# Optimization experiments

Hardware: AMD Instinct MI355X
Metric: run time of the kernel (lower is better)

The kernel has to match this reference:

```python
import jax, jax.numpy as jnp
import numpy as np

B, S, D, E, R = 8, 4096, 768, 8, 8

def setup_inputs() -> dict:
    key = jax.random.key(0)
    ks = jax.random.split(key, 9)
    sc = 0.02
    return {
        "x":  jax.random.normal(ks[0], (B, S, D), dtype=jnp.float32),
        "Wd": jax.random.normal(ks[1], (E, D, R), dtype=jnp.float32) * sc,
        "bd": jax.random.normal(ks[2], (E, R), dtype=jnp.float32) * sc,
        "Wm": jax.random.normal(ks[3], (E, R, R), dtype=jnp.float32) * sc,
        "bm": jax.random.normal(ks[4], (E, R), dtype=jnp.float32) * sc,
        "Wu": jax.random.normal(ks[5], (E, R, D), dtype=jnp.float32) * sc,
        "bu": jax.random.normal(ks[6], (E, D), dtype=jnp.float32) * sc,
        "Wg": jax.random.normal(ks[7], (D, E), dtype=jnp.float32) * sc,
        "bg": jax.random.normal(ks[8], (E,), dtype=jnp.float32) * sc,
    }

def reference(x, Wd, bd, Wm, bm, Wu, bu, Wg, bg):
    # Gating: softmax over experts. [B,S,E]
    gate = jax.nn.softmax(jnp.einsum('bsd,de->bse', x, Wg) + bg, axis=-1)
    # All experts batched as 3D GEMMs (dropout = identity, eval mode).
    h = jnp.einsum('bsd,edr->bser', x, Wd) + bd            # [B,S,E,R] down
    h = jnp.einsum('bser,erq->bseq', h, Wm) + bm           # [B,S,E,R] mid
    up = jnp.einsum('bser,erd->bsed', h, Wu) + bu          # [B,S,E,D] up
    # Weighted sum over experts.
    return jnp.einsum('bse,bsed->bsd', gate, up)
```

## Files before the change

kernel.cpp:

```cpp
#include <hip/hip_runtime.h>
#include <stdint.h>


typedef short bf16x8 __attribute__((ext_vector_type(8)));
typedef float f32x4 __attribute__((ext_vector_type(4)));

static __device__ __forceinline__ unsigned short f2bf(float f) {
  union { float f; uint32_t u; } v; v.f = f;
  return (unsigned short)((v.u + 0x7fffu + ((v.u >> 16) & 1u)) >> 16);
}

__global__ void prep_weights(const float* __restrict__ Wd, const float* __restrict__ Wg,
                             const float* __restrict__ Wu, const float* __restrict__ bu,
                             unsigned short* __restrict__ w1f, unsigned short* __restrict__ w2f) {
  int tid = blockIdx.x * 256 + threadIdx.x;
  const int N1 = 24 * 5 * 64 * 8;
  if (tid < N1) {
    int i    = tid & 7;
    int lane = (tid >> 3) & 63;
    int fk   = tid >> 9;
    int f = fk % 5, K0 = fk / 5;
    int k = K0 * 32 + (lane >> 4) * 8 + i;
    int j = f * 16 + (lane & 15);
    float val = 0.f;
    if (j < 64)      val = Wd[(size_t)(j >> 3) * 6144 + (size_t)k * 8 + (j & 7)];
    else if (j < 72) val = Wg[(size_t)k * 8 + (j - 64)];
    w1f[tid] = f2bf(val);
  } else {
    int t2 = tid - N1;
    if (t2 >= 48 * 3 * 64 * 8) return;
    int i    = t2 & 7;
    int lane = (t2 >> 3) & 63;
    int tk   = t2 >> 9;
    int K0 = tk % 3, T = tk / 3;
    int k = K0 * 32 + (lane >> 4) * 8 + i;
    int n = T * 16 + (lane & 15);
    float val = 0.f;
    if (k < 64)      val = Wu[(size_t)(k >> 3) * 6144 + (size_t)(k & 7) * 768 + n];
    else if (k < 72) val = bu[(size_t)(k - 64) * 768 + n];
    w2f[t2] = f2bf(val);
  }
}

__global__ __launch_bounds__(256, 4) void moba_fused(
    const float* __restrict__ x,
    const float* __restrict__ bd, const float* __restrict__ Wm,
    const float* __restrict__ bm, const float* __restrict__ bg,
    const unsigned short* __restrict__ w1f, const unsigned short* __restrict__ w2f,
    float* __restrict__ out) {
  __shared__ float Hs[2][32][81];
  __shared__ unsigned int g2s[32][52];

  const int tidx = threadIdx.x;
  const int lane = tidx & 63;
  const int wave = tidx >> 6;
  const int tg   = wave >> 1;
  const int kh   = wave & 1;
  const int arow = lane & 15;
  const int kgrp = lane >> 4;
  const int tok0 = blockIdx.x * 32;

  {
    const float* xrow = x + (size_t)(tok0 + tg * 16 + arow) * 768 + kh * 384 + kgrp * 8;
    f32x4 acc0 = {0,0,0,0}, acc1 = {0,0,0,0}, acc2 = {0,0,0,0}, acc3 = {0,0,0,0}, acc4 = {0,0,0,0};
    const bf16x8* w1v = (const bf16x8*)w1f + (size_t)(kh * 12) * 320 + lane;

    float4 xa[4][2];
    #pragma unroll
    for (int i = 0; i < 4; i++) {
      xa[i][0] = *(const float4*)(xrow + i * 32);
      xa[i][1] = *(const float4*)(xrow + i * 32 + 4);
    }
    #pragma unroll
    for (int i = 0; i < 12; i++) {
      float4 a0 = xa[i & 3][0];
      float4 a1 = xa[i & 3][1];
      if (i + 4 < 12) {
        xa[i & 3][0] = *(const float4*)(xrow + (i + 4) * 32);
        xa[i & 3][1] = *(const float4*)(xrow + (i + 4) * 32 + 4);
      }
      bf16x8 af;
      af[0] = (short)f2bf(a0.x); af[1] = (short)f2bf(a0.y);
      af[2] = (short)f2bf(a0.z); af[3] = (short)f2bf(a0.w);
      af[4] = (short)f2bf(a1.x); af[5] = (short)f2bf(a1.y);
      af[6] = (short)f2bf(a1.z); af[7] = (short)f2bf(a1.w);
      const bf16x8* bb = w1v + i * 320;
      acc0 = __builtin_amdgcn_mfma_f32_16x16x32_bf16(af, bb[0],   acc0, 0, 0, 0);
      acc1 = __builtin_amdgcn_mfma_f32_16x16x32_bf16(af, bb[64],  acc1, 0, 0, 0);
      acc2 = __builtin_amdgcn_mfma_f32_16x16x32_bf16(af, bb[128], acc2, 0, 0, 0);
      acc3 = __builtin_amdgcn_mfma_f32_16x16x32_bf16(af, bb[192], acc3, 0, 0, 0);
      acc4 = __builtin_amdgcn_mfma_f32_16x16x32_bf16(af, bb[256], acc4, 0, 0, 0);
    }
    int hr = tg * 16 + kgrp * 4;
    #pragma unroll
    for (int r = 0; r < 4; r++) {
      Hs[kh][hr + r][arow]      = acc0[r];
      Hs[kh][hr + r][16 + arow] = acc1[r];
      Hs[kh][hr + r][32 + arow] = acc2[r];
      Hs[kh][hr + r][48 + arow] = acc3[r];
      Hs[kh][hr + r][64 + arow] = acc4[r];
    }
  }
  __syncthreads();

  if (tidx < 128) {
    int t = tidx >> 2;
    int c = tidx & 3;
    float lg[8];
    float m = -1e30f;
    #pragma unroll
    for (int e = 0; e < 8; e++) {
      lg[e] = Hs[0][t][64 + e] + Hs[1][t][64 + e] + bg[e];
      m = fmaxf(m, lg[e]);
    }
    float den = 0.f;
    #pragma unroll
    for (int e = 0; e < 8; e++) { lg[e] = __expf(lg[e] - m); den += lg[e]; }
    float inv = 1.f / den;
    #pragma unroll
    for (int ee = 0; ee < 2; ee++) {
      int e = c * 2 + ee;
      float gate = lg[e] * inv;
      float h[8];
      #pragma unroll
      for (int r = 0; r < 8; r++)
        h[r] = Hs[0][t][e * 8 + r] + Hs[1][t][e * 8 + r] + bd[e * 8 + r];
      #pragma unroll
      for (int q = 0; q < 8; q += 2) {
        float h2a = bm[e * 8 + q], h2b = bm[e * 8 + q + 1];
        #pragma unroll
        for (int r = 0; r < 8; r++) {
          h2a += h[r] * Wm[e * 64 + r * 8 + q];
          h2b += h[r] * Wm[e * 64 + r * 8 + q + 1];
        }
        g2s[t][e * 4 + (q >> 1)] =
            (unsigned)f2bf(gate * h2a) | ((unsigned)f2bf(gate * h2b) << 16);
      }
    }
    g2s[t][32 + c] = (unsigned)f2bf(lg[c * 2] * inv) | ((unsigned)f2bf(lg[c * 2 + 1] * inv) << 16);
    g2s[t][36 + c * 3 + 0] = 0;
    g2s[t][36 + c * 3 + 1] = 0;
    g2s[t][36 + c * 3 + 2] = 0;
  }
  __syncthreads();

  bf16x8 a2_0 = *(const bf16x8*)&g2s[tg * 16 + arow][kgrp * 4];
  bf16x8 a2_1 = *(const bf16x8*)&g2s[tg * 16 + arow][16 + kgrp * 4];
  bf16x8 a2_2 = *(const bf16x8*)&g2s[tg * 16 + arow][32 + kgrp * 4];
  const bf16x8* w2v = (const bf16x8*)w2f + (size_t)(kh * 24) * 192 + lane;
  float* orow = out + (size_t)(tok0 + tg * 16 + kgrp * 4) * 768 + arow + kh * 384;

  bf16x8 pb[4][3];
  #pragma unroll
  for (int d = 0; d < 4; d++) {
    pb[d][0] = w2v[d * 192];
    pb[d][1] = w2v[d * 192 + 64];
    pb[d][2] = w2v[d * 192 + 128];
  }
  #pragma unroll
  for (int j = 0; j < 24; j++) {
    bf16x8 b0 = pb[j & 3][0], b1 = pb[j & 3][1], b2 = pb[j & 3][2];
    if (j + 4 < 24) {
      pb[j & 3][0] = w2v[(j + 4) * 192];
      pb[j & 3][1] = w2v[(j + 4) * 192 + 64];
      pb[j & 3][2] = w2v[(j + 4) * 192 + 128];
    }
    f32x4 c2 = {0,0,0,0};
    c2 = __builtin_amdgcn_mfma_f32_16x16x32_bf16(a2_0, b0, c2, 0, 0, 0);
    c2 = __builtin_amdgcn_mfma_f32_16x16x32_bf16(a2_1, b1, c2, 0, 0, 0);
    c2 = __builtin_amdgcn_mfma_f32_16x16x32_bf16(a2_2, b2, c2, 0, 0, 0);
    #pragma unroll
    for (int r = 0; r < 4; r++)
      orow[(size_t)r * 768 + j * 16] = c2[r];
  }
}

extern "C" void kernel_launch(void* const* d_in, const int* in_sizes, int n_in,
                              void* d_out, int out_size, void* d_ws, size_t ws_size,
                              hipStream_t stream) {
  const float* x  = (const float*)d_in[0];
  const float* Wd = (const float*)d_in[1];
  const float* bd = (const float*)d_in[2];
  const float* Wm = (const float*)d_in[3];
  const float* bm = (const float*)d_in[4];
  const float* Wu = (const float*)d_in[5];
  const float* bu = (const float*)d_in[6];
  const float* Wg = (const float*)d_in[7];
  const float* bg = (const float*)d_in[8];
  unsigned short* w1f = (unsigned short*)d_ws;
  unsigned short* w2f = w1f + 61440;

  prep_weights<<<528, 256, 0, stream>>>(Wd, Wg, Wu, bu, w1f, w2f);
  moba_fused<<<1024, 256, 0, stream>>>(x, bd, Wm, bm, bg, w1f, w2f, (float*)d_out);
}
```

Before: 57.72 us.

## Halve tokens per block, split K four ways across waves, use nontemporal stores

Each block now handles 16 tokens instead of 32. The four waves split the down-projection K dimension into quarters and the up-projection N dimension into quarters, and the grid doubles to 2048 blocks with launch bounds raised to 8 blocks per CU. The aim is more parallelism and occupancy for a memory-bound kernel, with output written through nontemporal stores to avoid cache pollution. In exchange, every block reloads the weight fragments, which doubles weight traffic per token, and only one wave runs the gating/mid stage.

```diff
diff --git a/kernel.cpp b/kernel.cpp
--- a/kernel.cpp
+++ b/kernel.cpp
@@ -42,28 +42,26 @@
   }
 }
 
-__global__ __launch_bounds__(256, 4) void moba_fused(
+__global__ __launch_bounds__(256, 8) void moba_fused(
     const float* __restrict__ x,
     const float* __restrict__ bd, const float* __restrict__ Wm,
     const float* __restrict__ bm, const float* __restrict__ bg,
     const unsigned short* __restrict__ w1f, const unsigned short* __restrict__ w2f,
     float* __restrict__ out) {
-  __shared__ float Hs[2][32][81];
-  __shared__ unsigned int g2s[32][52];
+  __shared__ float Hs[4][16][81];
+  __shared__ unsigned int g2s[16][52];
 
   const int tidx = threadIdx.x;
   const int lane = tidx & 63;
   const int wave = tidx >> 6;
-  const int tg   = wave >> 1;
-  const int kh   = wave & 1;
   const int arow = lane & 15;
   const int kgrp = lane >> 4;
-  const int tok0 = blockIdx.x * 32;
+  const int tok0 = blockIdx.x * 16;
 
   {
-    const float* xrow = x + (size_t)(tok0 + tg * 16 + arow) * 768 + kh * 384 + kgrp * 8;
+    const float* xrow = x + (size_t)(tok0 + arow) * 768 + wave * 192 + kgrp * 8;
     f32x4 acc0 = {0,0,0,0}, acc1 = {0,0,0,0}, acc2 = {0,0,0,0}, acc3 = {0,0,0,0}, acc4 = {0,0,0,0};
-    const bf16x8* w1v = (const bf16x8*)w1f + (size_t)(kh * 12) * 320 + lane;
+    const bf16x8* w1v = (const bf16x8*)w1f + (size_t)(wave * 6) * 320 + lane;
 
     float4 xa[4][2];
     #pragma unroll
@@ -72,10 +70,10 @@
       xa[i][1] = *(const float4*)(xrow + i * 32 + 4);
     }
     #pragma unroll
-    for (int i = 0; i < 12; i++) {
+    for (int i = 0; i < 6; i++) {
       float4 a0 = xa[i & 3][0];
       float4 a1 = xa[i & 3][1];
-      if (i + 4 < 12) {
+      if (i + 4 < 6) {
         xa[i & 3][0] = *(const float4*)(xrow + (i + 4) * 32);
         xa[i & 3][1] = *(const float4*)(xrow + (i + 4) * 32 + 4);
       }
@@ -91,26 +89,26 @@
       acc3 = __builtin_amdgcn_mfma_f32_16x16x32_bf16(af, bb[192], acc3, 0, 0, 0);
       acc4 = __builtin_amdgcn_mfma_f32_16x16x32_bf16(af, bb[256], acc4, 0, 0, 0);
     }
-    int hr = tg * 16 + kgrp * 4;
+    int hr = kgrp * 4;
     #pragma unroll
     for (int r = 0; r < 4; r++) {
-      Hs[kh][hr + r][arow]      = acc0[r];
-      Hs[kh][hr + r][16 + arow] = acc1[r];
-      Hs[kh][hr + r][32 + arow] = acc2[r];
-      Hs[kh][hr + r][48 + arow] = acc3[r];
-      Hs[kh][hr + r][64 + arow] = acc4[r];
+      Hs[wave][hr + r][arow]      = acc0[r];
+      Hs[wave][hr + r][16 + arow] = acc1[r];
+      Hs[wave][hr + r][32 + arow] = acc2[r];
+      Hs[wave][hr + r][48 + arow] = acc3[r];
+      Hs[wave][hr + r][64 + arow] = acc4[r];
     }
   }
   __syncthreads();
 
-  if (tidx < 128) {
+  if (tidx < 64) {
     int t = tidx >> 2;
     int c = tidx & 3;
     float lg[8];
     float m = -1e30f;
     #pragma unroll
     for (int e = 0; e < 8; e++) {
-      lg[e] = Hs[0][t][64 + e] + Hs[1][t][64 + e] + bg[e];
+      lg[e] = Hs[0][t][64 + e] + Hs[1][t][64 + e] + Hs[2][t][64 + e] + Hs[3][t][64 + e] + bg[e];
       m = fmaxf(m, lg[e]);
     }
     float den = 0.f;
@@ -124,7 +122,8 @@
       float h[8];
       #pragma unroll
       for (int r = 0; r < 8; r++)
-        h[r] = Hs[0][t][e * 8 + r] + Hs[1][t][e * 8 + r] + bd[e * 8 + r];
+        h[r] = Hs[0][t][e * 8 + r] + Hs[1][t][e * 8 + r] + Hs[2][t][e * 8 + r] +
+               Hs[3][t][e * 8 + r] + bd[e * 8 + r];
       #pragma unroll
       for (int q = 0; q < 8; q += 2) {
         float h2a = bm[e * 8 + q], h2b = bm[e * 8 + q + 1];
@@ -144,11 +143,11 @@
   }
   __syncthreads();
 
-  bf16x8 a2_0 = *(const bf16x8*)&g2s[tg * 16 + arow][kgrp * 4];
-  bf16x8 a2_1 = *(const bf16x8*)&g2s[tg * 16 + arow][16 + kgrp * 4];
-  bf16x8 a2_2 = *(const bf16x8*)&g2s[tg * 16 + arow][32 + kgrp * 4];
-  const bf16x8* w2v = (const bf16x8*)w2f + (size_t)(kh * 24) * 192 + lane;
-  float* orow = out + (size_t)(tok0 + tg * 16 + kgrp * 4) * 768 + arow + kh * 384;
+  bf16x8 a2_0 = *(const bf16x8*)&g2s[arow][kgrp * 4];
+  bf16x8 a2_1 = *(const bf16x8*)&g2s[arow][16 + kgrp * 4];
+  bf16x8 a2_2 = *(const bf16x8*)&g2s[arow][32 + kgrp * 4];
+  const bf16x8* w2v = (const bf16x8*)w2f + (size_t)(wave * 12) * 192 + lane;
+  float* orow = out + (size_t)(tok0 + kgrp * 4) * 768 + arow + wave * 192;
 
   bf16x8 pb[4][3];
   #pragma unroll
@@ -158,9 +157,9 @@
     pb[d][2] = w2v[d * 192 + 128];
   }
   #pragma unroll
-  for (int j = 0; j < 24; j++) {
+  for (int j = 0; j < 12; j++) {
     bf16x8 b0 = pb[j & 3][0], b1 = pb[j & 3][1], b2 = pb[j & 3][2];
-    if (j + 4 < 24) {
+    if (j + 4 < 12) {
       pb[j & 3][0] = w2v[(j + 4) * 192];
       pb[j & 3][1] = w2v[(j + 4) * 192 + 64];
       pb[j & 3][2] = w2v[(j + 4) * 192 + 128];
@@ -171,7 +170,7 @@
     c2 = __builtin_amdgcn_mfma_f32_16x16x32_bf16(a2_2, b2, c2, 0, 0, 0);
     #pragma unroll
     for (int r = 0; r < 4; r++)
-      orow[(size_t)r * 768 + j * 16] = c2[r];
+      __builtin_nontemporal_store(c2[r], orow + (size_t)r * 768 + j * 16);
   }
 }
 
@@ -191,5 +190,5 @@
   unsigned short* w2f = w1f + 61440;
 
   prep_weights<<<528, 256, 0, stream>>>(Wd, Wg, Wu, bu, w1f, w2f);
-  moba_fused<<<1024, 256, 0, stream>>>(x, bd, Wm, bm, bg, w1f, w2f, (float*)d_out);
+  moba_fused<<<2048, 256, 0, stream>>>(x, bd, Wm, bm, bg, w1f, w2f, (float*)d_out);
 }
```

Result: slower. 59.09 us (+2.4%).

## Split fused MoE kernel into gate/down kernel and up-projection kernel via workspace

Applied to the files above, without the earlier changes.

Splits the single fused kernel into two. The first computes the down projection, the gating and the mid projection, then writes the gated bf16 activations to a global workspace. The second reads those activations and runs the up-projection GEMM with swapped MFMA operands, so each lane stores a contiguous float4 and each wave covers 32 tokens by 192 columns. The aim is to get vectorized, coalesced output stores and to drop the shared-memory round trip and occupancy limit of the fused design, at the cost of an extra launch and an extra global write and read of the intermediate.

```diff
diff --git a/kernel.cpp b/kernel.cpp
--- a/kernel.cpp
+++ b/kernel.cpp
@@ -42,14 +42,12 @@
   }
 }
 
-__global__ __launch_bounds__(256, 4) void moba_fused(
+__global__ __launch_bounds__(256) void k1_g2(
     const float* __restrict__ x,
     const float* __restrict__ bd, const float* __restrict__ Wm,
     const float* __restrict__ bm, const float* __restrict__ bg,
-    const unsigned short* __restrict__ w1f, const unsigned short* __restrict__ w2f,
-    float* __restrict__ out) {
-  __shared__ float Hs[2][32][81];
-  __shared__ unsigned int g2s[32][52];
+    const unsigned short* __restrict__ w1f, unsigned int* __restrict__ g2) {
+  __shared__ float Hs[2][32][84];
 
   const int tidx = threadIdx.x;
   const int lane = tidx & 63;
@@ -106,6 +104,7 @@
   if (tidx < 128) {
     int t = tidx >> 2;
     int c = tidx & 3;
+    unsigned int* g2u = g2 + (size_t)(tok0 + t) * 48;
     float lg[8];
     float m = -1e30f;
     #pragma unroll
@@ -117,6 +116,7 @@
     #pragma unroll
     for (int e = 0; e < 8; e++) { lg[e] = __expf(lg[e] - m); den += lg[e]; }
     float inv = 1.f / den;
+    unsigned int hv[8];
     #pragma unroll
     for (int ee = 0; ee < 2; ee++) {
       int e = c * 2 + ee;
@@ -133,22 +133,41 @@
           h2a += h[r] * Wm[e * 64 + r * 8 + q];
           h2b += h[r] * Wm[e * 64 + r * 8 + q + 1];
         }
-        g2s[t][e * 4 + (q >> 1)] =
+        hv[ee * 4 + (q >> 1)] =
             (unsigned)f2bf(gate * h2a) | ((unsigned)f2bf(gate * h2b) << 16);
       }
     }
-    g2s[t][32 + c] = (unsigned)f2bf(lg[c * 2] * inv) | ((unsigned)f2bf(lg[c * 2 + 1] * inv) << 16);
-    g2s[t][36 + c * 3 + 0] = 0;
-    g2s[t][36 + c * 3 + 1] = 0;
-    g2s[t][36 + c * 3 + 2] = 0;
-  }
-  __syncthreads();
-
-  bf16x8 a2_0 = *(const bf16x8*)&g2s[tg * 16 + arow][kgrp * 4];
-  bf16x8 a2_1 = *(const bf16x8*)&g2s[tg * 16 + arow][16 + kgrp * 4];
-  bf16x8 a2_2 = *(const bf16x8*)&g2s[tg * 16 + arow][32 + kgrp * 4];
-  const bf16x8* w2v = (const bf16x8*)w2f + (size_t)(kh * 24) * 192 + lane;
-  float* orow = out + (size_t)(tok0 + tg * 16 + kgrp * 4) * 768 + arow + kh * 384;
+    *(uint4*)(g2u + 8 * c)     = make_uint4(hv[0], hv[1], hv[2], hv[3]);
+    *(uint4*)(g2u + 8 * c + 4) = make_uint4(hv[4], hv[5], hv[6], hv[7]);
+    g2u[32 + c] = (unsigned)f2bf(lg[c * 2] * inv) | ((unsigned)f2bf(lg[c * 2 + 1] * inv) << 16);
+    g2u[36 + c * 3 + 0] = 0;
+    g2u[36 + c * 3 + 1] = 0;
+    g2u[36 + c * 3 + 2] = 0;
+  }
+}
+
+__global__ __launch_bounds__(256) void k2_out(
+    const unsigned short* __restrict__ g2bf, const unsigned short* __restrict__ w2f,
+    float* __restrict__ out) {
+  const int tidx = threadIdx.x;
+  const int lane = tidx & 63;
+  const int wave = tidx >> 6;
+  const int arow = lane & 15;
+  const int kgrp = lane >> 4;
+  const int tok0 = blockIdx.x * 32;
+
+  const unsigned short* grow0 = g2bf + (size_t)(tok0 + arow) * 96 + kgrp * 8;
+  const unsigned short* grow1 = grow0 + 16 * 96;
+  bf16x8 a0_0 = *(const bf16x8*)(grow0);
+  bf16x8 a0_1 = *(const bf16x8*)(grow0 + 32);
+  bf16x8 a0_2 = *(const bf16x8*)(grow0 + 64);
+  bf16x8 a1_0 = *(const bf16x8*)(grow1);
+  bf16x8 a1_1 = *(const bf16x8*)(grow1 + 32);
+  bf16x8 a1_2 = *(const bf16x8*)(grow1 + 64);
+
+  const bf16x8* w2v = (const bf16x8*)w2f + (size_t)(wave * 12) * 192 + lane;
+  float* orow0 = out + (size_t)(tok0 + arow) * 768 + wave * 192 + kgrp * 4;
+  float* orow1 = orow0 + (size_t)16 * 768;
 
   bf16x8 pb[4][3];
   #pragma unroll
@@ -158,20 +177,22 @@
     pb[d][2] = w2v[d * 192 + 128];
   }
   #pragma unroll
-  for (int j = 0; j < 24; j++) {
+  for (int j = 0; j < 12; j++) {
     bf16x8 b0 = pb[j & 3][0], b1 = pb[j & 3][1], b2 = pb[j & 3][2];
-    if (j + 4 < 24) {
+    if (j + 4 < 12) {
       pb[j & 3][0] = w2v[(j + 4) * 192];
       pb[j & 3][1] = w2v[(j + 4) * 192 + 64];
       pb[j & 3][2] = w2v[(j + 4) * 192 + 128];
     }
-    f32x4 c2 = {0,0,0,0};
-    c2 = __builtin_amdgcn_mfma_f32_16x16x32_bf16(a2_0, b0, c2, 0, 0, 0);
-    c2 = __builtin_amdgcn_mfma_f32_16x16x32_bf16(a2_1, b1, c2, 0, 0, 0);
-    c2 = __builtin_amdgcn_mfma_f32_16x16x32_bf16(a2_2, b2, c2, 0, 0, 0);
-    #pragma unroll
-    for (int r = 0; r < 4; r++)
-      orow[(size_t)r * 768 + j * 16] = c2[r];
+    f32x4 c0 = {0,0,0,0}, c1 = {0,0,0,0};
+    c0 = __builtin_amdgcn_mfma_f32_16x16x32_bf16(b0, a0_0, c0, 0, 0, 0);
+    c1 = __builtin_amdgcn_mfma_f32_16x16x32_bf16(b0, a1_0, c1, 0, 0, 0);
+    c0 = __builtin_amdgcn_mfma_f32_16x16x32_bf16(b1, a0_1, c0, 0, 0, 0);
+    c1 = __builtin_amdgcn_mfma_f32_16x16x32_bf16(b1, a1_1, c1, 0, 0, 0);
+    c0 = __builtin_amdgcn_mfma_f32_16x16x32_bf16(b2, a0_2, c0, 0, 0, 0);
+    c1 = __builtin_amdgcn_mfma_f32_16x16x32_bf16(b2, a1_2, c1, 0, 0, 0);
+    *(f32x4*)(orow0 + j * 16) = c0;
+    *(f32x4*)(orow1 + j * 16) = c1;
   }
 }
 
@@ -189,7 +210,9 @@
   const float* bg = (const float*)d_in[8];
   unsigned short* w1f = (unsigned short*)d_ws;
   unsigned short* w2f = w1f + 61440;
+  unsigned int*   g2  = (unsigned int*)((char*)d_ws + 270336);
 
   prep_weights<<<528, 256, 0, stream>>>(Wd, Wg, Wu, bu, w1f, w2f);
-  moba_fused<<<1024, 256, 0, stream>>>(x, bd, Wm, bm, bg, w1f, w2f, (float*)d_out);
-}
+  k1_g2<<<1024, 256, 0, stream>>>(x, bd, Wm, bm, bg, w1f, g2);
+  k2_out<<<1024, 256, 0, stream>>>((const unsigned short*)g2, w2f, (float*)d_out);
+}
```

Measured after the change: 61.66 us. 6.8% more time.

## Transpose second-stage MFMA operands for vectorized output stores and weight reuse

Applied to the files above, without the earlier changes.

The up-projection stage swaps the MFMA A/B operands so each lane holds four consecutive output columns, which allows 16-byte float4 stores in place of scattered scalar stores. Each wave now covers both 16-token halves over a 192-column slice, so every weight fragment loaded serves two MFMAs and weight traffic per block is halved. The mid-stage results are packed into registers and written to shared memory as uint4, and the Hs row padding changes. Dropping the occupancy hint from launch_bounds lets the compiler allocate more registers, which may lower occupancy.

```diff
diff --git a/kernel.cpp b/kernel.cpp
--- a/kernel.cpp
+++ b/kernel.cpp
@@ -42,13 +42,13 @@
   }
 }
 
-__global__ __launch_bounds__(256, 4) void moba_fused(
+__global__ __launch_bounds__(256) void moba_fused(
     const float* __restrict__ x,
     const float* __restrict__ bd, const float* __restrict__ Wm,
     const float* __restrict__ bm, const float* __restrict__ bg,
     const unsigned short* __restrict__ w1f, const unsigned short* __restrict__ w2f,
     float* __restrict__ out) {
-  __shared__ float Hs[2][32][81];
+  __shared__ float Hs[2][32][84];
   __shared__ unsigned int g2s[32][52];
 
   const int tidx = threadIdx.x;
@@ -117,6 +117,7 @@
     #pragma unroll
     for (int e = 0; e < 8; e++) { lg[e] = __expf(lg[e] - m); den += lg[e]; }
     float inv = 1.f / den;
+    unsigned int hv[8];
     #pragma unroll
     for (int ee = 0; ee < 2; ee++) {
       int e = c * 2 + ee;
@@ -133,10 +134,12 @@
           h2a += h[r] * Wm[e * 64 + r * 8 + q];
           h2b += h[r] * Wm[e * 64 + r * 8 + q + 1];
         }
-        g2s[t][e * 4 + (q >> 1)] =
+        hv[ee * 4 + (q >> 1)] =
             (unsigned)f2bf(gate * h2a) | ((unsigned)f2bf(gate * h2b) << 16);
       }
     }
+    *(uint4*)&g2s[t][8 * c]     = make_uint4(hv[0], hv[1], hv[2], hv[3]);
+    *(uint4*)&g2s[t][8 * c + 4] = make_uint4(hv[4], hv[5], hv[6], hv[7]);
     g2s[t][32 + c] = (unsigned)f2bf(lg[c * 2] * inv) | ((unsigned)f2bf(lg[c * 2 + 1] * inv) << 16);
     g2s[t][36 + c * 3 + 0] = 0;
     g2s[t][36 + c * 3 + 1] = 0;
@@ -144,34 +147,41 @@
   }
   __syncthreads();
 
-  bf16x8 a2_0 = *(const bf16x8*)&g2s[tg * 16 + arow][kgrp * 4];
-  bf16x8 a2_1 = *(const bf16x8*)&g2s[tg * 16 + arow][16 + kgrp * 4];
-  bf16x8 a2_2 = *(const bf16x8*)&g2s[tg * 16 + arow][32 + kgrp * 4];
-  const bf16x8* w2v = (const bf16x8*)w2f + (size_t)(kh * 24) * 192 + lane;
-  float* orow = out + (size_t)(tok0 + tg * 16 + kgrp * 4) * 768 + arow + kh * 384;
-
-  bf16x8 pb[4][3];
+  bf16x8 a0_0 = *(const bf16x8*)&g2s[arow][kgrp * 4];
+  bf16x8 a0_1 = *(const bf16x8*)&g2s[arow][16 + kgrp * 4];
+  bf16x8 a0_2 = *(const bf16x8*)&g2s[arow][32 + kgrp * 4];
+  bf16x8 a1_0 = *(const bf16x8*)&g2s[16 + arow][kgrp * 4];
+  bf16x8 a1_1 = *(const bf16x8*)&g2s[16 + arow][16 + kgrp * 4];
+  bf16x8 a1_2 = *(const bf16x8*)&g2s[16 + arow][32 + kgrp * 4];
+
+  const bf16x8* w2v = (const bf16x8*)w2f + (size_t)(wave * 12) * 192 + lane;
+  float* orow0 = out + (size_t)(tok0 + arow) * 768 + wave * 192 + kgrp * 4;
+  float* orow1 = orow0 + (size_t)16 * 768;
+
+  bf16x8 pb[2][3];
   #pragma unroll
-  for (int d = 0; d < 4; d++) {
+  for (int d = 0; d < 2; d++) {
     pb[d][0] = w2v[d * 192];
     pb[d][1] = w2v[d * 192 + 64];
     pb[d][2] = w2v[d * 192 + 128];
   }
   #pragma unroll
-  for (int j = 0; j < 24; j++) {
-    bf16x8 b0 = pb[j & 3][0], b1 = pb[j & 3][1], b2 = pb[j & 3][2];
-    if (j + 4 < 24) {
-      pb[j & 3][0] = w2v[(j + 4) * 192];
-      pb[j & 3][1] = w2v[(j + 4) * 192 + 64];
-      pb[j & 3][2] = w2v[(j + 4) * 192 + 128];
-    }
-    f32x4 c2 = {0,0,0,0};
-    c2 = __builtin_amdgcn_mfma_f32_16x16x32_bf16(a2_0, b0, c2, 0, 0, 0);
-    c2 = __builtin_amdgcn_mfma_f32_16x16x32_bf16(a2_1, b1, c2, 0, 0, 0);
-    c2 = __builtin_amdgcn_mfma_f32_16x16x32_bf16(a2_2, b2, c2, 0, 0, 0);
-    #pragma unroll
-    for (int r = 0; r < 4; r++)
-      orow[(size_t)r * 768 + j * 16] = c2[r];
+  for (int j = 0; j < 12; j++) {
+    bf16x8 b0 = pb[j & 1][0], b1 = pb[j & 1][1], b2 = pb[j & 1][2];
+    if (j + 2 < 12) {
+      pb[j & 1][0] = w2v[(j + 2) * 192];
+      pb[j & 1][1] = w2v[(j + 2) * 192 + 64];
+      pb[j & 1][2] = w2v[(j + 2) * 192 + 128];
+    }
+    f32x4 c0 = {0,0,0,0}, c1 = {0,0,0,0};
+    c0 = __builtin_amdgcn_mfma_f32_16x16x32_bf16(b0, a0_0, c0, 0, 0, 0);
+    c1 = __builtin_amdgcn_mfma_f32_16x16x32_bf16(b0, a1_0, c1, 0, 0, 0);
+    c0 = __builtin_amdgcn_mfma_f32_16x16x32_bf16(b1, a0_1, c0, 0, 0, 0);
+    c1 = __builtin_amdgcn_mfma_f32_16x16x32_bf16(b1, a1_1, c1, 0, 0, 0);
+    c0 = __builtin_amdgcn_mfma_f32_16x16x32_bf16(b2, a0_2, c0, 0, 0, 0);
+    c1 = __builtin_amdgcn_mfma_f32_16x16x32_bf16(b2, a1_2, c1, 0, 0, 0);
+    *(f32x4*)(orow0 + j * 16) = c0;
+    *(f32x4*)(orow1 + j * 16) = c1;
   }
 }
 
```

After: 57.50 us. No clear change (-0.4%).
